# Kernel optimization log

Measured on AMD Instinct MI355X. Metric: run time of the kernel, lower is better.

Reference implementation:

```python
import jax, jax.numpy as jnp
import numpy as np

D_MODEL = 768
NUM_HEADS = 12
HEAD_DIM = D_MODEL // NUM_HEADS
BATCH = 1
SEQ = 4096


def setup_inputs() -> dict:
    key = jax.random.key(0)
    ks = jax.random.split(key, 11)
    s = 0.02
    return {
        "q": jax.random.normal(ks[0], (BATCH, SEQ, D_MODEL), jnp.float32),
        "k": jax.random.normal(ks[1], (BATCH, SEQ, D_MODEL), jnp.float32),
        "v": jax.random.normal(ks[2], (BATCH, SEQ, D_MODEL), jnp.float32),
        "Wq": jax.random.normal(ks[3], (D_MODEL, D_MODEL), jnp.float32) * s,
        "bq": jnp.zeros((D_MODEL,), jnp.float32),
        "Wk": jax.random.normal(ks[4], (D_MODEL, D_MODEL), jnp.float32) * s,
        "bk": jnp.zeros((D_MODEL,), jnp.float32),
        "Wv": jax.random.normal(ks[5], (D_MODEL, D_MODEL), jnp.float32) * s,
        "bv": jnp.zeros((D_MODEL,), jnp.float32),
        "Wo": jax.random.normal(ks[6], (D_MODEL, D_MODEL), jnp.float32) * s,
        "bo": jnp.zeros((D_MODEL,), jnp.float32),
    }


def reference(q, k, v, Wq, bq, Wk, bk, Wv, bv, Wo, bo):
    B, S, D = q.shape
    H, Hd = NUM_HEADS, HEAD_DIM
    # linear projections (torch Linear: x @ W.T + b)
    qh = (q @ Wq.T + bq).reshape(B, S, H, Hd).transpose(0, 2, 1, 3)  # [B,H,S,Hd]
    kh = (k @ Wk.T + bk).reshape(B, S, H, Hd).transpose(0, 2, 1, 3)
    vh = (v @ Wv.T + bv).reshape(B, S, H, Hd).transpose(0, 2, 1, 3)
    scale = 1.0 / jnp.sqrt(jnp.asarray(Hd, qh.dtype))
    scores = jnp.einsum("bhsd,bhtd->bhst", qh, kh) * scale  # [B,H,S,S]
    weights = jax.nn.softmax(scores, axis=-1)
    attn = jnp.einsum("bhst,bhtd->bhsd", weights, vh)  # [B,H,S,Hd]
    attn = attn.transpose(0, 2, 1, 3).reshape(B, S, D)
    return attn @ Wo.T + bo
```

## Files before the change

### kernel.cpp

```cpp
#include <hip/hip_runtime.h>

#define S_LEN 4096
#define DMODEL 768
#define NHEAD 12
#define HD 64

typedef __bf16 bf16x8 __attribute__((ext_vector_type(8)));
typedef __bf16 bf16x4 __attribute__((ext_vector_type(4)));
typedef float f32x4 __attribute__((ext_vector_type(4)));
typedef float f32x16 __attribute__((ext_vector_type(16)));
typedef unsigned short u16x8 __attribute__((ext_vector_type(8)));

#if __has_builtin(__builtin_amdgcn_exp2f)
#define EXP2F(x) __builtin_amdgcn_exp2f(x)
#else
#define EXP2F(x) exp2f(x)
#endif

#define MFMA32(a, b, c) __builtin_amdgcn_mfma_f32_32x32x16_bf16(a, b, c, 0, 0, 0)

__device__ __forceinline__ unsigned short f2bf(float f) {
  unsigned int u = __float_as_uint(f);
  u += 0x7fffu + ((u >> 16) & 1u);
  return (unsigned short)(u >> 16);
}

__device__ __forceinline__ void gload_lds16(const void* g, void* l) {
  __builtin_amdgcn_global_load_lds(
      (__attribute__((address_space(1))) void*)g,
      (__attribute__((address_space(3))) void*)l, 16, 0, 0);
}

struct CvtArgs {
  const float* src[7];
  unsigned short* dst[7];
  int n[7];
};

__global__ __launch_bounds__(256) void cvt_kernel(CvtArgs a) {
  const int seg = blockIdx.y;
  const int n = a.n[seg];
  const int i = (blockIdx.x * 256 + threadIdx.x) * 8;
  if (i >= n) return;
  const float* s = a.src[seg] + i;
  u16x8 o;
#pragma unroll
  for (int j = 0; j < 8; ++j) o[j] = f2bf(s[j]);
  *reinterpret_cast<u16x8*>(a.dst[seg] + i) = o;
}

struct QkvArgs {
  const unsigned short* A[3];
  const unsigned short* W[3];
  const float* bias[3];
  unsigned short* dst[3];
  float scale[3];
};

__global__ __launch_bounds__(256) void qkv_gemm(QkvArgs a) {
  __shared__ unsigned char lds[32768];
  const int z = blockIdx.z;
  const unsigned short* __restrict__ A = a.A[z];
  const unsigned short* __restrict__ B = a.W[z];
  const float* __restrict__ bias = a.bias[z];
  unsigned short* __restrict__ dst = a.dst[z];
  const float scale = a.scale[z];

  const int tid = threadIdx.x;
  const int lane = tid & 63;
  const int w = tid >> 6;
  const int wr = w >> 1, wc = w & 1;
  const int c = lane & 15, g = lane >> 4;
  const int m0 = blockIdx.x * 128;
  const int n0 = blockIdx.y * 128;

  f32x4 acc[4][4] = {};

  for (int kt = 0; kt < DMODEL / 64; ++kt) {
#pragma unroll
    for (int p = 0; p < 4; ++p) {
      const int te = p * 256 + tid;
      const int row = te >> 3;
      const int sb = ((te & 7) * 16) ^ ((row & 7) << 4);
      gload_lds16(A + (size_t)(m0 + row) * DMODEL + kt * 64 + (sb >> 1), &lds[te * 16]);
      gload_lds16(B + (size_t)(n0 + row) * DMODEL + kt * 64 + (sb >> 1), &lds[16384 + te * 16]);
    }
    __syncthreads();

    bf16x8 af[4][2], bfr[4][2];
#pragma unroll
    for (int mb = 0; mb < 4; ++mb)
#pragma unroll
      for (int ks = 0; ks < 2; ++ks) {
        const int row = wr * 64 + mb * 16 + c;
        const int byte = (ks * 64 + g * 16) ^ ((row & 7) << 4);
        af[mb][ks] = *reinterpret_cast<const bf16x8*>(&lds[row * 128 + byte]);
      }
#pragma unroll
    for (int nb = 0; nb < 4; ++nb)
#pragma unroll
      for (int ks = 0; ks < 2; ++ks) {
        const int row = wc * 64 + nb * 16 + c;
        const int byte = (ks * 64 + g * 16) ^ ((row & 7) << 4);
        bfr[nb][ks] = *reinterpret_cast<const bf16x8*>(&lds[16384 + row * 128 + byte]);
      }
    __builtin_amdgcn_s_setprio(1);
#pragma unroll
    for (int ks = 0; ks < 2; ++ks)
#pragma unroll
      for (int mb = 0; mb < 4; ++mb)
#pragma unroll
        for (int nb = 0; nb < 4; ++nb)
          acc[mb][nb] = __builtin_amdgcn_mfma_f32_16x16x32_bf16(
              af[mb][ks], bfr[nb][ks], acc[mb][nb], 0, 0, 0);
    __builtin_amdgcn_s_setprio(0);
    __syncthreads();
  }

#pragma unroll
  for (int mb = 0; mb < 4; ++mb) {
#pragma unroll
    for (int nb = 0; nb < 4; ++nb) {
      const int n = n0 + wc * 64 + nb * 16 + c;
      const float bv = bias[n];
#pragma unroll
      for (int r = 0; r < 4; ++r) {
        const int m = m0 + wr * 64 + mb * 16 + g * 4 + r;
        const float v = (acc[mb][nb][r] + bv) * scale;
        const int hh = n >> 6, hd = n & 63;
        if (z != 2) {
          dst[((size_t)hh * S_LEN + m) * HD + hd] = f2bf(v);
        } else {
          dst[((size_t)hh * HD + hd) * S_LEN + m] = f2bf(v);
        }
      }
    }
  }
}

__global__ __launch_bounds__(256) void gemm_out(
    const unsigned short* __restrict__ A, const unsigned short* __restrict__ B,
    const float* __restrict__ bias, float* __restrict__ dst) {
  __shared__ unsigned char lds[32768];
  const int tid = threadIdx.x;
  const int lane = tid & 63;
  const int w = tid >> 6;
  const int wr = w >> 1, wc = w & 1;
  const int c = lane & 15, g = lane >> 4;
  const int m0 = blockIdx.x * 128;
  const int n0 = blockIdx.y * 128;

  f32x4 acc[4][4] = {};

  for (int kt = 0; kt < DMODEL / 64; ++kt) {
#pragma unroll
    for (int p = 0; p < 4; ++p) {
      const int te = p * 256 + tid;
      const int row = te >> 3;
      const int sb = ((te & 7) * 16) ^ ((row & 7) << 4);
      gload_lds16(A + (size_t)(m0 + row) * DMODEL + kt * 64 + (sb >> 1), &lds[te * 16]);
      gload_lds16(B + (size_t)(n0 + row) * DMODEL + kt * 64 + (sb >> 1), &lds[16384 + te * 16]);
    }
    __syncthreads();

    bf16x8 af[4][2], bfr[4][2];
#pragma unroll
    for (int mb = 0; mb < 4; ++mb)
#pragma unroll
      for (int ks = 0; ks < 2; ++ks) {
        const int row = wr * 64 + mb * 16 + c;
        const int byte = (ks * 64 + g * 16) ^ ((row & 7) << 4);
        af[mb][ks] = *reinterpret_cast<const bf16x8*>(&lds[row * 128 + byte]);
      }
#pragma unroll
    for (int nb = 0; nb < 4; ++nb)
#pragma unroll
      for (int ks = 0; ks < 2; ++ks) {
        const int row = wc * 64 + nb * 16 + c;
        const int byte = (ks * 64 + g * 16) ^ ((row & 7) << 4);
        bfr[nb][ks] = *reinterpret_cast<const bf16x8*>(&lds[16384 + row * 128 + byte]);
      }
    __builtin_amdgcn_s_setprio(1);
#pragma unroll
    for (int ks = 0; ks < 2; ++ks)
#pragma unroll
      for (int mb = 0; mb < 4; ++mb)
#pragma unroll
        for (int nb = 0; nb < 4; ++nb)
          acc[mb][nb] = __builtin_amdgcn_mfma_f32_16x16x32_bf16(
              af[mb][ks], bfr[nb][ks], acc[mb][nb], 0, 0, 0);
    __builtin_amdgcn_s_setprio(0);
    __syncthreads();
  }

#pragma unroll
  for (int mb = 0; mb < 4; ++mb)
#pragma unroll
    for (int nb = 0; nb < 4; ++nb) {
      const int n = n0 + wc * 64 + nb * 16 + c;
      const float bv = bias[n];
#pragma unroll
      for (int r = 0; r < 4; ++r) {
        const int m = m0 + wr * 64 + mb * 16 + g * 4 + r;
        dst[(size_t)m * DMODEL + n] = acc[mb][nb][r] + bv;
      }
    }
}

__global__ __launch_bounds__(128) void attn_kernel(
    const unsigned short* __restrict__ qh,
    const unsigned short* __restrict__ kh,
    const unsigned short* __restrict__ vt,
    unsigned short* __restrict__ attn) {
  __shared__ unsigned char lds[32768];
  const int tid = threadIdx.x;
  const int lane = tid & 63;
  const int w = tid >> 6;
  const int c5 = lane & 31;
  const int h2 = lane >> 5;
  const int hh = blockIdx.y;
  const int qw = blockIdx.x * 64 + w * 32;

  bf16x8 qa[4];
#pragma unroll
  for (int ks = 0; ks < 4; ++ks)
    qa[ks] = *reinterpret_cast<const bf16x8*>(
        qh + ((size_t)hh * S_LEN + qw + c5) * HD + ks * 16 + h2 * 8);

  const int row0 = tid >> 3;
  const int sb = ((tid & 7) * 16) ^ ((row0 & 7) << 4);
  const unsigned short* ksrc = kh + ((size_t)hh * S_LEN + row0) * HD + (sb >> 1);
  const unsigned short* vsrc = vt + ((size_t)hh * HD + row0) * S_LEN + (sb >> 1);
  const int dK = tid * 16;

#pragma unroll
  for (int p = 0; p < 4; ++p) {
    gload_lds16(ksrc + p * 16 * HD, &lds[dK + p * 2048]);
    gload_lds16(vsrc + (size_t)p * 16 * S_LEN, &lds[8192 + dK + p * 2048]);
  }
  ksrc += 64 * HD;
  vsrc += 64;
  __syncthreads();

  f32x16 accO[2] = {};
  float rs0 = 0.f, rs1 = 0.f, rs2 = 0.f, rs3 = 0.f;
  const int swz = (c5 & 7) << 4;

  int buf = 0;
  for (int kt = 0; kt < S_LEN / 64; ++kt) {
    if (kt + 1 < S_LEN / 64) {
      const int nb_ = (buf ^ 1) * 16384;
#pragma unroll
      for (int p = 0; p < 4; ++p) {
        gload_lds16(ksrc + p * 16 * HD, &lds[nb_ + dK + p * 2048]);
        gload_lds16(vsrc + (size_t)p * 16 * S_LEN, &lds[nb_ + 8192 + dK + p * 2048]);
      }
      ksrc += 64 * HD;
      vsrc += 64;
    }
    const unsigned char* Kb = &lds[buf * 16384];
    const unsigned char* Vb = &lds[buf * 16384 + 8192];

    f32x16 s0 = {}, s1 = {};
    __builtin_amdgcn_s_setprio(1);
#pragma unroll
    for (int ks = 0; ks < 4; ++ks) {
      const int byte = (ks * 32 + h2 * 16) ^ swz;
      const bf16x8 k0 = *reinterpret_cast<const bf16x8*>(&Kb[c5 * 128 + byte]);
      const bf16x8 k1 = *reinterpret_cast<const bf16x8*>(&Kb[(32 + c5) * 128 + byte]);
      s0 = MFMA32(k0, qa[ks], s0);
      s1 = MFMA32(k1, qa[ks], s1);
    }
    __builtin_amdgcn_s_setprio(0);

    bf16x8 p00, p01, p10, p11;
#pragma unroll
    for (int r = 0; r < 8; ++r) {
      const float e0 = EXP2F(s0[r]);
      const float e1 = EXP2F(s0[8 + r]);
      const float e2 = EXP2F(s1[r]);
      const float e3 = EXP2F(s1[8 + r]);
      rs0 += e0; rs1 += e1; rs2 += e2; rs3 += e3;
      p00[r] = (__bf16)e0;
      p01[r] = (__bf16)e1;
      p10[r] = (__bf16)e2;
      p11[r] = (__bf16)e3;
    }

    __builtin_amdgcn_s_setprio(1);
#pragma unroll
    for (int t = 0; t < 2; ++t)
#pragma unroll
      for (int ss = 0; ss < 2; ++ss) {
        const bf16x8 pb = t ? (ss ? p11 : p10) : (ss ? p01 : p00);
        const int off = t * 64 + ss * 32 + h2 * 8;
#pragma unroll
        for (int dt = 0; dt < 2; ++dt) {
          const int rowb = (dt * 32 + c5) * 128;
          const bf16x4 lo = *reinterpret_cast<const bf16x4*>(&Vb[rowb + (off ^ swz)]);
          const bf16x4 hi = *reinterpret_cast<const bf16x4*>(&Vb[rowb + ((off + 16) ^ swz)]);
          accO[dt] = MFMA32(__builtin_shufflevector(lo, hi, 0, 1, 2, 3, 4, 5, 6, 7),
                            pb, accO[dt]);
        }
      }
    __builtin_amdgcn_s_setprio(0);

    __syncthreads();
    buf ^= 1;
  }

  float rsA = (rs0 + rs1) + (rs2 + rs3);
  rsA += __shfl_xor(rsA, 32);
  const float inv = 1.f / rsA;

#pragma unroll
  for (int dt = 0; dt < 2; ++dt)
#pragma unroll
    for (int rr = 0; rr < 4; ++rr) {
      bf16x4 o;
#pragma unroll
      for (int j = 0; j < 4; ++j) o[j] = (__bf16)(accO[dt][rr * 4 + j] * inv);
      const int d = dt * 32 + rr * 8 + h2 * 4;
      *reinterpret_cast<bf16x4*>(
          attn + (size_t)(qw + c5) * DMODEL + hh * HD + d) = o;
    }
}

extern "C" void kernel_launch(void* const* d_in, const int* in_sizes, int n_in,
                              void* d_out, int out_size, void* d_ws, size_t ws_size,
                              hipStream_t stream) {
  (void)in_sizes; (void)n_in; (void)out_size;
  const float* q  = (const float*)d_in[0];
  const float* k  = (const float*)d_in[1];
  const float* v  = (const float*)d_in[2];
  const float* Wq = (const float*)d_in[3];
  const float* bq = (const float*)d_in[4];
  const float* Wk = (const float*)d_in[5];
  const float* bk = (const float*)d_in[6];
  const float* Wv = (const float*)d_in[7];
  const float* bv = (const float*)d_in[8];
  const float* Wo = (const float*)d_in[9];
  const float* bo = (const float*)d_in[10];
  float* out = (float*)d_out;

  const size_t SD = (size_t)S_LEN * DMODEL;
  const size_t DD = (size_t)DMODEL * DMODEL;
  if (ws_size < (7 * SD + 4 * DD) * 2) return;

  unsigned short* ws   = (unsigned short*)d_ws;
  unsigned short* qbf  = ws;
  unsigned short* kbf  = qbf + SD;
  unsigned short* vbf  = kbf + SD;
  unsigned short* wqb  = vbf + SD;
  unsigned short* wkb  = wqb + DD;
  unsigned short* wvb  = wkb + DD;
  unsigned short* wob  = wvb + DD;
  unsigned short* qhb  = wob + DD;
  unsigned short* khb  = qhb + SD;
  unsigned short* vtb  = khb + SD;
  unsigned short* attb = vtb + SD;

  CvtArgs ca;
  ca.src[0] = q;  ca.dst[0] = qbf; ca.n[0] = (int)SD;
  ca.src[1] = k;  ca.dst[1] = kbf; ca.n[1] = (int)SD;
  ca.src[2] = v;  ca.dst[2] = vbf; ca.n[2] = (int)SD;
  ca.src[3] = Wq; ca.dst[3] = wqb; ca.n[3] = (int)DD;
  ca.src[4] = Wk; ca.dst[4] = wkb; ca.n[4] = (int)DD;
  ca.src[5] = Wv; ca.dst[5] = wvb; ca.n[5] = (int)DD;
  ca.src[6] = Wo; ca.dst[6] = wob; ca.n[6] = (int)DD;
  cvt_kernel<<<dim3(1536, 7), 256, 0, stream>>>(ca);

  QkvArgs qa;
  qa.A[0] = qbf; qa.W[0] = wqb; qa.bias[0] = bq; qa.dst[0] = qhb;
  qa.scale[0] = 0.18033688011112042f;
  qa.A[1] = kbf; qa.W[1] = wkb; qa.bias[1] = bk; qa.dst[1] = khb;
  qa.scale[1] = 1.0f;
  qa.A[2] = vbf; qa.W[2] = wvb; qa.bias[2] = bv; qa.dst[2] = vtb;
  qa.scale[2] = 1.0f;
  qkv_gemm<<<dim3(32, 6, 3), 256, 0, stream>>>(qa);

  attn_kernel<<<dim3(S_LEN / 64, NHEAD), 128, 0, stream>>>(qhb, khb, vtb, attb);

  gemm_out<<<dim3(32, 6), 256, 0, stream>>>(attb, wob, bo, out);
}
```

Before: 150.8 us.

## Split attention KV range in two with combine kernel and permuted V layout

The attention kernel now splits the key/value sequence into two halves across blockIdx.z. Each half writes an unnormalized fp16 partial output and a row sum, and a new combine kernel adds the halves, normalizes, and writes bf16. The V-transpose store permutes sequence indices so the P·V loop can do one 16-byte LDS read instead of two 8-byte reads. The loop barriers are replaced with explicit waitcnt and s_barrier so the next tile's loads overlap compute. This doubles the grid to improve CU occupancy, at the cost of an extra kernel launch and the partial-result traffic; the workspace buffers are reused for the partials.

```diff
diff --git a/kernel.cpp b/kernel.cpp
--- a/kernel.cpp
+++ b/kernel.cpp
@@ -10,6 +10,8 @@
 typedef float f32x4 __attribute__((ext_vector_type(4)));
 typedef float f32x16 __attribute__((ext_vector_type(16)));
 typedef unsigned short u16x8 __attribute__((ext_vector_type(8)));
+typedef unsigned short u16x4 __attribute__((ext_vector_type(4)));
+typedef _Float16 f16x4 __attribute__((ext_vector_type(4)));
 
 #if __has_builtin(__builtin_amdgcn_exp2f)
 #define EXP2F(x) __builtin_amdgcn_exp2f(x)
@@ -131,7 +133,8 @@
         if (z != 2) {
           dst[((size_t)hh * S_LEN + m) * HD + hd] = f2bf(v);
         } else {
-          dst[((size_t)hh * HD + hd) * S_LEN + m] = f2bf(v);
+          const int mp = (m & ~12) | ((m & 4) << 1) | ((m & 8) >> 1);
+          dst[((size_t)hh * HD + hd) * S_LEN + mp] = f2bf(v);
         }
       }
     }
@@ -210,8 +213,9 @@
 __global__ __launch_bounds__(128) void attn_kernel(
     const unsigned short* __restrict__ qh,
     const unsigned short* __restrict__ kh,
-    const unsigned short* __restrict__ vt,
-    unsigned short* __restrict__ attn) {
+    const unsigned short* __restrict__ vtp,
+    _Float16* __restrict__ pacc,
+    float* __restrict__ prs) {
   __shared__ unsigned char lds[32768];
   const int tid = threadIdx.x;
   const int lane = tid & 63;
@@ -219,7 +223,10 @@
   const int c5 = lane & 31;
   const int h2 = lane >> 5;
   const int hh = blockIdx.y;
+  const int split = blockIdx.z;
   const int qw = blockIdx.x * 64 + w * 32;
+  const int kv0 = split * (S_LEN / 2);
+  const int NKT = (S_LEN / 2) / 64;
 
   bf16x8 qa[4];
 #pragma unroll
@@ -229,8 +236,8 @@
 
   const int row0 = tid >> 3;
   const int sb = ((tid & 7) * 16) ^ ((row0 & 7) << 4);
-  const unsigned short* ksrc = kh + ((size_t)hh * S_LEN + row0) * HD + (sb >> 1);
-  const unsigned short* vsrc = vt + ((size_t)hh * HD + row0) * S_LEN + (sb >> 1);
+  const unsigned short* ksrc = kh + ((size_t)hh * S_LEN + kv0 + row0) * HD + (sb >> 1);
+  const unsigned short* vsrc = vtp + ((size_t)hh * HD + row0) * S_LEN + kv0 + (sb >> 1);
   const int dK = tid * 16;
 
 #pragma unroll
@@ -240,27 +247,12 @@
   }
   ksrc += 64 * HD;
   vsrc += 64;
-  __syncthreads();
 
   f32x16 accO[2] = {};
   float rs0 = 0.f, rs1 = 0.f, rs2 = 0.f, rs3 = 0.f;
   const int swz = (c5 & 7) << 4;
 
-  int buf = 0;
-  for (int kt = 0; kt < S_LEN / 64; ++kt) {
-    if (kt + 1 < S_LEN / 64) {
-      const int nb_ = (buf ^ 1) * 16384;
-#pragma unroll
-      for (int p = 0; p < 4; ++p) {
-        gload_lds16(ksrc + p * 16 * HD, &lds[nb_ + dK + p * 2048]);
-        gload_lds16(vsrc + (size_t)p * 16 * S_LEN, &lds[nb_ + 8192 + dK + p * 2048]);
-      }
-      ksrc += 64 * HD;
-      vsrc += 64;
-    }
-    const unsigned char* Kb = &lds[buf * 16384];
-    const unsigned char* Vb = &lds[buf * 16384 + 8192];
-
+  auto compute = [&](const unsigned char* Kb, const unsigned char* Vb) {
     f32x16 s0 = {}, s1 = {};
     __builtin_amdgcn_s_setprio(1);
 #pragma unroll
@@ -293,37 +285,78 @@
 #pragma unroll
       for (int ss = 0; ss < 2; ++ss) {
         const bf16x8 pb = t ? (ss ? p11 : p10) : (ss ? p01 : p00);
-        const int off = t * 64 + ss * 32 + h2 * 8;
+        const int byte = (t * 64 + ss * 32 + h2 * 16) ^ swz;
 #pragma unroll
         for (int dt = 0; dt < 2; ++dt) {
-          const int rowb = (dt * 32 + c5) * 128;
-          const bf16x4 lo = *reinterpret_cast<const bf16x4*>(&Vb[rowb + (off ^ swz)]);
-          const bf16x4 hi = *reinterpret_cast<const bf16x4*>(&Vb[rowb + ((off + 16) ^ swz)]);
-          accO[dt] = MFMA32(__builtin_shufflevector(lo, hi, 0, 1, 2, 3, 4, 5, 6, 7),
-                            pb, accO[dt]);
+          const bf16x8 va = *reinterpret_cast<const bf16x8*>(
+              &Vb[(dt * 32 + c5) * 128 + byte]);
+          accO[dt] = MFMA32(va, pb, accO[dt]);
         }
       }
     __builtin_amdgcn_s_setprio(0);
-
-    __syncthreads();
+  };
+
+  int buf = 0;
+  for (int kt = 0; kt < NKT - 1; ++kt) {
+    const int nb_ = (buf ^ 1) * 16384;
+#pragma unroll
+    for (int p = 0; p < 4; ++p) {
+      gload_lds16(ksrc + p * 16 * HD, &lds[nb_ + dK + p * 2048]);
+      gload_lds16(vsrc + (size_t)p * 16 * S_LEN, &lds[nb_ + 8192 + dK + p * 2048]);
+    }
+    ksrc += 64 * HD;
+    vsrc += 64;
+    asm volatile("s_waitcnt vmcnt(8)" ::: "memory");
+    __builtin_amdgcn_sched_barrier(0);
+    __builtin_amdgcn_s_barrier();
+    __builtin_amdgcn_sched_barrier(0);
+    compute(&lds[buf * 16384], &lds[buf * 16384 + 8192]);
+    asm volatile("s_waitcnt lgkmcnt(0)" ::: "memory");
+    __builtin_amdgcn_sched_barrier(0);
+    __builtin_amdgcn_s_barrier();
     buf ^= 1;
   }
+  asm volatile("s_waitcnt vmcnt(0)" ::: "memory");
+  __builtin_amdgcn_sched_barrier(0);
+  __builtin_amdgcn_s_barrier();
+  __builtin_amdgcn_sched_barrier(0);
+  compute(&lds[buf * 16384], &lds[buf * 16384 + 8192]);
 
   float rsA = (rs0 + rs1) + (rs2 + rs3);
   rsA += __shfl_xor(rsA, 32);
-  const float inv = 1.f / rsA;
-
+  const size_t hqbase = ((size_t)split * NHEAD + hh) * S_LEN + qw + c5;
+  if (h2 == 0) prs[hqbase] = rsA * 0.015625f;
 #pragma unroll
   for (int dt = 0; dt < 2; ++dt)
 #pragma unroll
     for (int rr = 0; rr < 4; ++rr) {
-      bf16x4 o;
-#pragma unroll
-      for (int j = 0; j < 4; ++j) o[j] = (__bf16)(accO[dt][rr * 4 + j] * inv);
-      const int d = dt * 32 + rr * 8 + h2 * 4;
-      *reinterpret_cast<bf16x4*>(
-          attn + (size_t)(qw + c5) * DMODEL + hh * HD + d) = o;
-    }
+      f16x4 o;
+#pragma unroll
+      for (int j = 0; j < 4; ++j)
+        o[j] = (_Float16)(accO[dt][rr * 4 + j] * 0.015625f);
+      *reinterpret_cast<f16x4*>(
+          pacc + hqbase * 64 + dt * 32 + rr * 8 + h2 * 4) = o;
+    }
+}
+
+__global__ __launch_bounds__(256) void combine_kernel(
+    const _Float16* __restrict__ pacc, const float* __restrict__ prs,
+    unsigned short* __restrict__ attb) {
+  const int idx = blockIdx.x * 256 + threadIdx.x;
+  const int hq = idx >> 4;
+  const int d4 = (idx & 15) * 4;
+  const int h = hq >> 12;
+  const int q = hq & 4095;
+  const size_t o0 = (size_t)hq * 64 + d4;
+  const size_t o1 = o0 + (size_t)NHEAD * S_LEN * 64;
+  const f16x4 av = *reinterpret_cast<const f16x4*>(pacc + o0);
+  const f16x4 bv = *reinterpret_cast<const f16x4*>(pacc + o1);
+  const float inv = 1.f / (prs[hq] + prs[hq + NHEAD * S_LEN]);
+  u16x4 ov;
+#pragma unroll
+  for (int j = 0; j < 4; ++j)
+    ov[j] = f2bf(((float)av[j] + (float)bv[j]) * inv);
+  *reinterpret_cast<u16x4*>(attb + (size_t)q * DMODEL + h * HD + d4) = ov;
 }
 
 extern "C" void kernel_launch(void* const* d_in, const int* in_sizes, int n_in,
@@ -360,6 +393,9 @@
   unsigned short* vtb  = khb + SD;
   unsigned short* attb = vtb + SD;
 
+  _Float16* pacc = (_Float16*)qbf;
+  float*    prs  = (float*)wqb;
+
   CvtArgs ca;
   ca.src[0] = q;  ca.dst[0] = qbf; ca.n[0] = (int)SD;
   ca.src[1] = k;  ca.dst[1] = kbf; ca.n[1] = (int)SD;
@@ -379,7 +415,11 @@
   qa.scale[2] = 1.0f;
   qkv_gemm<<<dim3(32, 6, 3), 256, 0, stream>>>(qa);
 
-  attn_kernel<<<dim3(S_LEN / 64, NHEAD), 128, 0, stream>>>(qhb, khb, vtb, attb);
+  attn_kernel<<<dim3(S_LEN / 64, NHEAD, 2), 128, 0, stream>>>(
+      qhb, khb, vtb, pacc, prs);
+
+  combine_kernel<<<dim3((NHEAD * S_LEN * 16) / 256), 256, 0, stream>>>(
+      pacc, prs, attb);
 
   gemm_out<<<dim3(32, 6), 256, 0, stream>>>(attb, wob, bo, out);
 }
```

Measured after the change: 156.2 us. 1.04x slower.
